# Optimization experiments

Hardware: AMD Instinct MI355X
Metric: run time of the kernel (lower is better)

Reference implementation:

```python
import jax, jax.numpy as jnp
import numpy as np

BT, HID, E, INTER, TOPK = 256, 2048, 8, 4096, 2

def setup_inputs() -> dict:
    key = jax.random.key(0)
    k1, k2, k3, k4, k5 = jax.random.split(key, 5)
    hidden_states = jax.random.normal(k1, (BT, HID), dtype=jnp.float32)
    expert_routing_table = jax.random.randint(k2, (BT, TOPK), 0, E, dtype=jnp.int64)
    router_weights = jax.random.uniform(k3, (BT, TOPK), dtype=jnp.float32)
    # learned params, scaled like trained weights
    w13_weight = jax.random.normal(k4, (E, 2 * INTER, HID), dtype=jnp.float32) * 0.02
    w2_weight = jax.random.normal(k5, (E, HID, INTER), dtype=jnp.float32) * 0.02
    return {
        "hidden_states": hidden_states,
        "expert_routing_table": expert_routing_table,
        "router_weights": router_weights,
        "w13_weight": w13_weight,
        "w2_weight": w2_weight,
    }

def reference(hidden_states, expert_routing_table, router_weights, w13_weight, w2_weight):
    bt, hidden_dim = hidden_states.shape
    num_experts = w13_weight.shape[0]
    inter = w2_weight.shape[2]
    sel = expert_routing_table  # [bt, top_k], ep_shift = 0
    # scatter router weights into dense [bt, E] (torch scatter_ set semantics)
    rows = jnp.arange(bt)[:, None]
    padded_weights = jnp.zeros((bt, num_experts), dtype=hidden_states.dtype)
    padded_weights = padded_weights.at[rows, sel].set(router_weights)
    # dense per-expert up/gate projection: [bt, E, 2*inter]
    up_gate = jnp.einsum('th,efh->tef', hidden_states, w13_weight)
    up_gate = up_gate.reshape(bt, num_experts, 2, inter)
    up_states = up_gate[:, :, 0, :]
    gate_states = up_gate[:, :, 1, :]
    cur = jax.nn.silu(up_states) * gate_states  # [bt, E, inter]
    # down projection + masked routed-weight sum over experts
    down = jnp.einsum('tei,ehi->teh', cur, w2_weight)  # [bt, E, hidden]
    final = jnp.einsum('teh,te->th', down, padded_weights)
    return final.reshape(-1, hidden_dim)
```

## Files before the change

### kernel.cpp

```cpp
#include <hip/hip_runtime.h>

#define BT 256
#define HID 2048
#define NE 8
#define INTER 4096

typedef short short8 __attribute__((ext_vector_type(8)));
typedef float f32x4 __attribute__((ext_vector_type(4)));

__device__ inline unsigned short f2bf(float f){
  unsigned int u = __float_as_uint(f);
  u += 0x7fff + ((u >> 16) & 1);
  return (unsigned short)(u >> 16);
}
__device__ inline unsigned int pk2(float x, float y){
  return (unsigned int)f2bf(x) | ((unsigned int)f2bf(y) << 16);
}
__device__ inline short8 cvt8(float4 a, float4 b){
  union { unsigned int u[4]; short8 s; } r;
  r.u[0] = pk2(a.x, a.y); r.u[1] = pk2(a.z, a.w);
  r.u[2] = pk2(b.x, b.y); r.u[3] = pk2(b.z, b.w);
  return r.s;
}

__device__ inline void glds16(const void* g, void* l){
  __builtin_amdgcn_global_load_lds(
      (const __attribute__((address_space(1))) unsigned int*)g,
      (__attribute__((address_space(3))) unsigned int*)l, 16, 0, 0);
}

__device__ inline short8 fragf(const float* tile, int row, int kbase){
  int cp = (kbase >> 3) ^ (row & 7);
  const float4* p = (const float4*)(tile + row*64 + cp*8);
  return cvt8(p[0], p[1]);
}
__device__ inline short8 fragh(const unsigned short* tile, int row, int kbase){
  int cp = (kbase >> 3) ^ (row & 7);
  return *(const short8*)(tile + row*64 + cp*8);
}

__global__ void routing_kernel(const int* __restrict__ sel, const float* __restrict__ rw,
                               int* counts, int* bases, int* tokl, float* wtl){
  __shared__ int cnt[NE]; __shared__ int bs[NE]; __shared__ int cur[NE];
  int t = threadIdx.x;
  if (t < NE) cnt[t] = 0;
  __syncthreads();
  int s0 = sel[2*t], s1 = sel[2*t+1];
  float w0 = rw[2*t], w1 = rw[2*t+1];
  bool dup = (s0 == s1);
  atomicAdd(&cnt[s1], 1);
  if (!dup) atomicAdd(&cnt[s0], 1);
  __syncthreads();
  if (t == 0){ int a = 0; for (int e = 0; e < NE; e++){ bs[e] = a; cur[e] = a; a += cnt[e]; } }
  __syncthreads();
  int slot = atomicAdd(&cur[s1], 1); tokl[slot] = t; wtl[slot] = w1;
  if (!dup){ slot = atomicAdd(&cur[s0], 1); tokl[slot] = t; wtl[slot] = w0; }
  if (t < NE){ counts[t] = cnt[t]; bases[t] = bs[t]; }
}

__global__ __launch_bounds__(256, 3) void gemm1_kernel(
    const float* __restrict__ hs, const float* __restrict__ w13,
    const int* __restrict__ counts, const int* __restrict__ bases,
    const int* __restrict__ tokl, unsigned short* __restrict__ cur)
{
  const int e = blockIdx.z;
  const int cnt = counts[e];
  const int mtile = blockIdx.y;
  if (mtile * 64 >= cnt) return;
  const int f0 = blockIdx.x * 64;
  const int base = bases[e];
  const int tid = threadIdx.x;

  __shared__ __align__(16) float As[64*64];
  __shared__ __align__(16) float Bs[128*64];

  const float* gA[4]; int offA[4];
#pragma unroll
  for (int r = 0; r < 4; r++){
    int off = r*4096 + tid*16;
    int row = off >> 8, b = off & 255;
    int cp = b >> 5, half = (b >> 4) & 1;
    int col = ((cp ^ (row & 7)) * 8) + half*4;
    int slot = mtile*64 + row; if (slot >= cnt) slot = cnt - 1;
    gA[r] = hs + (size_t)tokl[base + slot] * HID + col;
    offA[r] = off;
  }
  const float* gB[8]; int offB[8];
#pragma unroll
  for (int r = 0; r < 8; r++){
    int off = r*4096 + tid*16;
    int row = off >> 8, b = off & 255;
    int cp = b >> 5, half = (b >> 4) & 1;
    int col = ((cp ^ (row & 7)) * 8) + half*4;
    int wrow = (row < 64) ? (f0 + row) : (INTER + f0 + row - 64);
    gB[r] = w13 + (size_t)e * 2*INTER*HID + (size_t)wrow * HID + col;
    offB[r] = off;
  }

  const int wv = tid >> 6, wm = wv >> 1, wn = wv & 1;
  const int lane = tid & 63;
  const int lrow = lane & 15, quad = lane >> 4;

  f32x4 acc[2][2][2];
#pragma unroll
  for (int s=0;s<2;s++) for (int mt=0;mt<2;mt++) for (int nt=0;nt<2;nt++)
    acc[s][mt][nt] = (f32x4){0.f,0.f,0.f,0.f};

  for (int k0 = 0; k0 < HID; k0 += 64){
#pragma unroll
    for (int r = 0; r < 4; r++) glds16(gA[r] + k0, (char*)As + offA[r]);
#pragma unroll
    for (int r = 0; r < 8; r++) glds16(gB[r] + k0, (char*)Bs + offB[r]);
    __syncthreads();
#pragma unroll
    for (int ks = 0; ks < 64; ks += 32){
      int kb = ks + quad*8;
      short8 a[2], bb[2][2];
#pragma unroll
      for (int mt=0;mt<2;mt++) a[mt] = fragf(As, wm*32 + mt*16 + lrow, kb);
#pragma unroll
      for (int s=0;s<2;s++)
#pragma unroll
        for (int nt=0;nt<2;nt++)
          bb[s][nt] = fragf(Bs, s*64 + wn*32 + nt*16 + lrow, kb);
#pragma unroll
      for (int s=0;s<2;s++)
#pragma unroll
        for (int mt=0;mt<2;mt++)
#pragma unroll
          for (int nt=0;nt<2;nt++)
            acc[s][mt][nt] = __builtin_amdgcn_mfma_f32_16x16x32_bf16(
                a[mt], bb[s][nt], acc[s][mt][nt], 0,0,0);
    }
    __syncthreads();
  }

#pragma unroll
  for (int mt = 0; mt < 2; mt++){
#pragma unroll
    for (int reg = 0; reg < 4; reg++){
      int m = mtile*64 + wm*32 + mt*16 + quad*4 + reg;
      if (m >= cnt) continue;
      size_t rowoff = (size_t)(base + m) * INTER;
#pragma unroll
      for (int nt = 0; nt < 2; nt++){
        int i = f0 + wn*32 + nt*16 + lrow;
        float up   = acc[0][mt][nt][reg];
        float gate = acc[1][mt][nt][reg];
        float sv = up / (1.f + __expf(-up));
        cur[rowoff + i] = f2bf(sv * gate);
      }
    }
  }
}

__global__ __launch_bounds__(256, 4) void gemm2_kernel(
    const unsigned short* __restrict__ cur, const float* __restrict__ w2,
    const int* __restrict__ counts, const int* __restrict__ bases,
    const int* __restrict__ tokl, const float* __restrict__ wtl,
    float* __restrict__ out)
{
  const int e  = blockIdx.z >> 1;
  const int kb0 = (blockIdx.z & 1) * 2048;
  const int cnt = counts[e];
  const int mtile = blockIdx.y;
  if (mtile * 64 >= cnt) return;
  const int h0 = blockIdx.x * 32;
  const int base = bases[e];
  const int tid = threadIdx.x;

  __shared__ __align__(16) unsigned short Ah[64*64];
  __shared__ __align__(16) float Bs[32*64];

  const unsigned short* gA[2]; int offA[2];
#pragma unroll
  for (int r = 0; r < 2; r++){
    int off = r*4096 + tid*16;
    int row = off >> 7;
    int cp = (off >> 4) & 7;
    int col = (cp ^ (row & 7)) * 8;
    int slot = mtile*64 + row; if (slot >= cnt) slot = cnt - 1;
    gA[r] = cur + (size_t)(base + slot) * INTER + kb0 + col;
    offA[r] = off;
  }
  const float* gB[2]; int offB[2];
#pragma unroll
  for (int r = 0; r < 2; r++){
    int off = r*4096 + tid*16;
    int row = off >> 8, b = off & 255;
    int cp = b >> 5, half = (b >> 4) & 1;
    int col = ((cp ^ (row & 7)) * 8) + half*4;
    gB[r] = w2 + (size_t)e * HID * INTER + (size_t)(h0 + row) * INTER + kb0 + col;
    offB[r] = off;
  }

  const int wv = tid >> 6, wm = wv >> 1, wn = wv & 1;
  const int lane = tid & 63;
  const int lrow = lane & 15, quad = lane >> 4;

  f32x4 acc[2];
  acc[0] = (f32x4){0.f,0.f,0.f,0.f};
  acc[1] = (f32x4){0.f,0.f,0.f,0.f};

  for (int k0 = 0; k0 < 2048; k0 += 64){
#pragma unroll
    for (int r = 0; r < 2; r++) glds16(gA[r] + k0, (char*)Ah + offA[r]);
#pragma unroll
    for (int r = 0; r < 2; r++) glds16(gB[r] + k0, (char*)Bs + offB[r]);
    __syncthreads();
#pragma unroll
    for (int ks = 0; ks < 64; ks += 32){
      int kb = ks + quad*8;
      short8 a[2], b;
#pragma unroll
      for (int mt=0;mt<2;mt++) a[mt] = fragh(Ah, wm*32 + mt*16 + lrow, kb);
      b = fragf(Bs, wn*16 + lrow, kb);
#pragma unroll
      for (int mt=0;mt<2;mt++)
        acc[mt] = __builtin_amdgcn_mfma_f32_16x16x32_bf16(a[mt], b, acc[mt], 0,0,0);
    }
    __syncthreads();
  }

#pragma unroll
  for (int mt = 0; mt < 2; mt++){
#pragma unroll
    for (int reg = 0; reg < 4; reg++){
      int m = mtile*64 + wm*32 + mt*16 + quad*4 + reg;
      if (m >= cnt) continue;
      int tk  = tokl[base + m];
      float w = wtl[base + m];
      int h = h0 + wn*16 + lrow;
      atomicAdd(&out[(size_t)tk * HID + h], w * acc[mt][reg]);
    }
  }
}

extern "C" void kernel_launch(void* const* d_in, const int* in_sizes, int n_in,
                              void* d_out, int out_size, void* d_ws, size_t ws_size,
                              hipStream_t stream){
  const float* hs  = (const float*)d_in[0];
  const int*   sel = (const int*)d_in[1];
  const float* rw  = (const float*)d_in[2];
  const float* w13 = (const float*)d_in[3];
  const float* w2  = (const float*)d_in[4];
  float* out = (float*)d_out;
  char* ws = (char*)d_ws;

  int* counts = (int*)ws;
  int* bases  = counts + 8;
  int* tokl   = bases + 8;
  float* wtl  = (float*)(tokl + 512);
  unsigned short* cur = (unsigned short*)(ws + 8192);

  hipMemsetAsync(d_out, 0, (size_t)BT * HID * sizeof(float), stream);
  routing_kernel<<<1, 256, 0, stream>>>(sel, rw, counts, bases, tokl, wtl);
  dim3 g1(INTER/64, 4, NE);
  gemm1_kernel<<<g1, 256, 0, stream>>>(hs, w13, counts, bases, tokl, cur);
  dim3 g2(HID/32, 4, NE*2);
  gemm2_kernel<<<g2, 256, 0, stream>>>(cur, w2, counts, bases, tokl, wtl, out);
}
```

Measured before the change: 924.7 us.

## Pre-gather bf16 activations, double-buffer GEMM k-loops, enlarge M tiles to 128

A new gather kernel copies the routed token rows into a contiguous bf16 buffer, so gemm1 loads compact bf16 A tiles instead of indirect fp32 rows. Both GEMMs now use 128-row M tiles with k-step 32 and a two-stage LDS double buffer, using explicit vmcnt waits and raw barriers so loads overlap MFMA work. gemm2 drops the K split and computes 64-wide H tiles, which halves the atomic traffic per output element. In exchange there is an extra launch, lower occupancy, and row reads past cnt that rely on workspace padding.

```diff
diff --git a/kernel.cpp b/kernel.cpp
--- a/kernel.cpp
+++ b/kernel.cpp
@@ -12,6 +12,9 @@
   unsigned int u = __float_as_uint(f);
   u += 0x7fff + ((u >> 16) & 1);
   return (unsigned short)(u >> 16);
+}
+__device__ inline ushort4 f2bf4(float4 v){
+  ushort4 b; b.x=f2bf(v.x); b.y=f2bf(v.y); b.z=f2bf(v.z); b.w=f2bf(v.w); return b;
 }
 __device__ inline unsigned int pk2(float x, float y){
   return (unsigned int)f2bf(x) | ((unsigned int)f2bf(y) << 16);
@@ -29,15 +32,8 @@
       (__attribute__((address_space(3))) unsigned int*)l, 16, 0, 0);
 }
 
-__device__ inline short8 fragf(const float* tile, int row, int kbase){
-  int cp = (kbase >> 3) ^ (row & 7);
-  const float4* p = (const float4*)(tile + row*64 + cp*8);
-  return cvt8(p[0], p[1]);
-}
-__device__ inline short8 fragh(const unsigned short* tile, int row, int kbase){
-  int cp = (kbase >> 3) ^ (row & 7);
-  return *(const short8*)(tile + row*64 + cp*8);
-}
+#define WAIT_BARRIER(N) asm volatile("s_waitcnt vmcnt(" #N ")\n\ts_barrier" ::: "memory")
+#define RAW_BARRIER()   asm volatile("s_barrier" ::: "memory")
 
 __global__ void routing_kernel(const int* __restrict__ sel, const float* __restrict__ rw,
                                int* counts, int* bases, int* tokl, float* wtl){
@@ -58,88 +54,121 @@
   if (t < NE){ counts[t] = cnt[t]; bases[t] = bs[t]; }
 }
 
-__global__ __launch_bounds__(256, 3) void gemm1_kernel(
-    const float* __restrict__ hs, const float* __restrict__ w13,
+__global__ void gather_kernel(const float* __restrict__ hs,
+                              const int* __restrict__ counts, const int* __restrict__ bases,
+                              const int* __restrict__ tokl, unsigned short* __restrict__ hsg){
+  int b = blockIdx.x;
+  int tot = bases[NE-1] + counts[NE-1];
+  if (b >= tot) return;
+  const float* src = hs + (size_t)tokl[b] * HID;
+  unsigned short* dst = hsg + (size_t)b * HID;
+  int t = threadIdx.x;
+  float4 v0 = *(const float4*)(src + t*8);
+  float4 v1 = *(const float4*)(src + t*8 + 4);
+  *(ushort4*)(dst + t*8)     = f2bf4(v0);
+  *(ushort4*)(dst + t*8 + 4) = f2bf4(v1);
+}
+
+__global__ __launch_bounds__(256, 2) void gemm1_kernel(
+    const unsigned short* __restrict__ hsg, const float* __restrict__ w13,
     const int* __restrict__ counts, const int* __restrict__ bases,
-    const int* __restrict__ tokl, unsigned short* __restrict__ cur)
+    unsigned short* __restrict__ cur)
 {
   const int e = blockIdx.z;
   const int cnt = counts[e];
   const int mtile = blockIdx.y;
-  if (mtile * 64 >= cnt) return;
+  if (mtile * 128 >= cnt) return;
   const int f0 = blockIdx.x * 64;
   const int base = bases[e];
   const int tid = threadIdx.x;
 
-  __shared__ __align__(16) float As[64*64];
-  __shared__ __align__(16) float Bs[128*64];
-
-  const float* gA[4]; int offA[4];
+  __shared__ __align__(16) unsigned short Abuf[2][128*32];
+  __shared__ __align__(16) float          Bbuf[2][128*32];
+
+  const unsigned short* aG[2]; int aL[2];
+#pragma unroll
+  for (int r = 0; r < 2; r++){
+    int off = r*4096 + tid*16;
+    int row = off >> 6;
+    int gpos = (off >> 4) & 3;
+    int gglob = gpos ^ ((row >> 1) & 3);
+    aG[r] = hsg + (size_t)(base + mtile*128 + row) * HID + gglob*8;
+    aL[r] = off;
+  }
+  const float* bG[4]; int bL[4];
+  const size_t ebase = (size_t)e * 2*INTER*HID;
 #pragma unroll
   for (int r = 0; r < 4; r++){
     int off = r*4096 + tid*16;
-    int row = off >> 8, b = off & 255;
-    int cp = b >> 5, half = (b >> 4) & 1;
-    int col = ((cp ^ (row & 7)) * 8) + half*4;
-    int slot = mtile*64 + row; if (slot >= cnt) slot = cnt - 1;
-    gA[r] = hs + (size_t)tokl[base + slot] * HID + col;
-    offA[r] = off;
-  }
-  const float* gB[8]; int offB[8];
-#pragma unroll
-  for (int r = 0; r < 8; r++){
-    int off = r*4096 + tid*16;
-    int row = off >> 8, b = off & 255;
-    int cp = b >> 5, half = (b >> 4) & 1;
-    int col = ((cp ^ (row & 7)) * 8) + half*4;
+    int row = off >> 7;
+    int gpos = (off >> 4) & 7;
+    int gglob = gpos ^ (row & 7);
     int wrow = (row < 64) ? (f0 + row) : (INTER + f0 + row - 64);
-    gB[r] = w13 + (size_t)e * 2*INTER*HID + (size_t)wrow * HID + col;
-    offB[r] = off;
+    bG[r] = w13 + ebase + (size_t)wrow * HID + gglob*4;
+    bL[r] = off;
   }
 
   const int wv = tid >> 6, wm = wv >> 1, wn = wv & 1;
   const int lane = tid & 63;
   const int lrow = lane & 15, quad = lane >> 4;
 
-  f32x4 acc[2][2][2];
-#pragma unroll
-  for (int s=0;s<2;s++) for (int mt=0;mt<2;mt++) for (int nt=0;nt<2;nt++)
+  f32x4 acc[2][4][2];
+#pragma unroll
+  for (int s=0;s<2;s++) for (int mt=0;mt<4;mt++) for (int nt=0;nt<2;nt++)
     acc[s][mt][nt] = (f32x4){0.f,0.f,0.f,0.f};
 
-  for (int k0 = 0; k0 < HID; k0 += 64){
-#pragma unroll
-    for (int r = 0; r < 4; r++) glds16(gA[r] + k0, (char*)As + offA[r]);
-#pragma unroll
-    for (int r = 0; r < 8; r++) glds16(gB[r] + k0, (char*)Bs + offB[r]);
-    __syncthreads();
-#pragma unroll
-    for (int ks = 0; ks < 64; ks += 32){
-      int kb = ks + quad*8;
-      short8 a[2], bb[2][2];
-#pragma unroll
-      for (int mt=0;mt<2;mt++) a[mt] = fragf(As, wm*32 + mt*16 + lrow, kb);
-#pragma unroll
-      for (int s=0;s<2;s++)
-#pragma unroll
-        for (int nt=0;nt<2;nt++)
-          bb[s][nt] = fragf(Bs, s*64 + wn*32 + nt*16 + lrow, kb);
-#pragma unroll
-      for (int s=0;s<2;s++)
-#pragma unroll
-        for (int mt=0;mt<2;mt++)
-#pragma unroll
-          for (int nt=0;nt<2;nt++)
-            acc[s][mt][nt] = __builtin_amdgcn_mfma_f32_16x16x32_bf16(
-                a[mt], bb[s][nt], acc[s][mt][nt], 0,0,0);
-    }
-    __syncthreads();
-  }
-
-#pragma unroll
-  for (int mt = 0; mt < 2; mt++){
+  auto issue = [&](int t2, int p){
+    int k0 = t2 * 32;
+#pragma unroll
+    for (int r = 0; r < 2; r++) glds16(aG[r] + k0, (char*)&Abuf[p][0] + aL[r]);
+#pragma unroll
+    for (int r = 0; r < 4; r++) glds16(bG[r] + k0, (char*)&Bbuf[p][0] + bL[r]);
+  };
+  auto compute = [&](int p){
+    const unsigned short* A = &Abuf[p][0];
+    const float* B = &Bbuf[p][0];
+    short8 a[4], b[2][2];
+#pragma unroll
+    for (int mt = 0; mt < 4; mt++){
+      int row = wm*64 + mt*16 + lrow;
+      a[mt] = *(const short8*)(A + row*32 + ((quad ^ ((row>>1)&3)) * 8));
+    }
+#pragma unroll
+    for (int s = 0; s < 2; s++)
+#pragma unroll
+      for (int nt = 0; nt < 2; nt++){
+        int row = s*64 + wn*32 + nt*16 + lrow;
+        int g0 = (2*quad) ^ (row & 7), g1 = (2*quad+1) ^ (row & 7);
+        float4 x = *(const float4*)(B + row*32 + g0*4);
+        float4 y = *(const float4*)(B + row*32 + g1*4);
+        b[s][nt] = cvt8(x, y);
+      }
+#pragma unroll
+    for (int s = 0; s < 2; s++)
+#pragma unroll
+      for (int mt = 0; mt < 4; mt++)
+#pragma unroll
+        for (int nt = 0; nt < 2; nt++)
+          acc[s][mt][nt] = __builtin_amdgcn_mfma_f32_16x16x32_bf16(
+              a[mt], b[s][nt], acc[s][mt][nt], 0,0,0);
+  };
+
+  const int T = HID / 32;
+  issue(0, 0); issue(1, 1);
+  for (int t = 0; t < T-1; t++){
+    WAIT_BARRIER(6);
+    compute(t & 1);
+    RAW_BARRIER();
+    if (t + 2 < T) issue(t + 2, t & 1);
+  }
+  WAIT_BARRIER(0);
+  compute((T-1) & 1);
+
+#pragma unroll
+  for (int mt = 0; mt < 4; mt++){
 #pragma unroll
     for (int reg = 0; reg < 4; reg++){
-      int m = mtile*64 + wm*32 + mt*16 + quad*4 + reg;
+      int m = mtile*128 + wm*64 + mt*16 + quad*4 + reg;
       if (m >= cnt) continue;
       size_t rowoff = (size_t)(base + m) * INTER;
 #pragma unroll
@@ -154,84 +183,109 @@
   }
 }
 
-__global__ __launch_bounds__(256, 4) void gemm2_kernel(
+__global__ __launch_bounds__(256, 2) void gemm2_kernel(
     const unsigned short* __restrict__ cur, const float* __restrict__ w2,
     const int* __restrict__ counts, const int* __restrict__ bases,
     const int* __restrict__ tokl, const float* __restrict__ wtl,
     float* __restrict__ out)
 {
-  const int e  = blockIdx.z >> 1;
-  const int kb0 = (blockIdx.z & 1) * 2048;
+  const int e = blockIdx.z;
   const int cnt = counts[e];
   const int mtile = blockIdx.y;
-  if (mtile * 64 >= cnt) return;
-  const int h0 = blockIdx.x * 32;
+  if (mtile * 128 >= cnt) return;
+  const int h0 = blockIdx.x * 64;
   const int base = bases[e];
   const int tid = threadIdx.x;
 
-  __shared__ __align__(16) unsigned short Ah[64*64];
-  __shared__ __align__(16) float Bs[32*64];
-
-  const unsigned short* gA[2]; int offA[2];
+  __shared__ __align__(16) unsigned short Abuf[2][128*32];
+  __shared__ __align__(16) float          Bbuf[2][64*32];
+
+  const unsigned short* aG[2]; int aL[2];
+#pragma unroll
+  for (int r = 0; r < 2; r++){
+    int off = r*4096 + tid*16;
+    int row = off >> 6;
+    int gpos = (off >> 4) & 3;
+    int gglob = gpos ^ ((row >> 1) & 3);
+    aG[r] = cur + (size_t)(base + mtile*128 + row) * INTER + gglob*8;
+    aL[r] = off;
+  }
+  const float* bG[2]; int bL[2];
+  const size_t ebase = (size_t)e * HID * INTER;
 #pragma unroll
   for (int r = 0; r < 2; r++){
     int off = r*4096 + tid*16;
     int row = off >> 7;
-    int cp = (off >> 4) & 7;
-    int col = (cp ^ (row & 7)) * 8;
-    int slot = mtile*64 + row; if (slot >= cnt) slot = cnt - 1;
-    gA[r] = cur + (size_t)(base + slot) * INTER + kb0 + col;
-    offA[r] = off;
-  }
-  const float* gB[2]; int offB[2];
-#pragma unroll
-  for (int r = 0; r < 2; r++){
-    int off = r*4096 + tid*16;
-    int row = off >> 8, b = off & 255;
-    int cp = b >> 5, half = (b >> 4) & 1;
-    int col = ((cp ^ (row & 7)) * 8) + half*4;
-    gB[r] = w2 + (size_t)e * HID * INTER + (size_t)(h0 + row) * INTER + kb0 + col;
-    offB[r] = off;
+    int gpos = (off >> 4) & 7;
+    int gglob = gpos ^ (row & 7);
+    bG[r] = w2 + ebase + (size_t)(h0 + row) * INTER + gglob*4;
+    bL[r] = off;
   }
 
   const int wv = tid >> 6, wm = wv >> 1, wn = wv & 1;
   const int lane = tid & 63;
   const int lrow = lane & 15, quad = lane >> 4;
 
-  f32x4 acc[2];
-  acc[0] = (f32x4){0.f,0.f,0.f,0.f};
-  acc[1] = (f32x4){0.f,0.f,0.f,0.f};
-
-  for (int k0 = 0; k0 < 2048; k0 += 64){
-#pragma unroll
-    for (int r = 0; r < 2; r++) glds16(gA[r] + k0, (char*)Ah + offA[r]);
-#pragma unroll
-    for (int r = 0; r < 2; r++) glds16(gB[r] + k0, (char*)Bs + offB[r]);
-    __syncthreads();
-#pragma unroll
-    for (int ks = 0; ks < 64; ks += 32){
-      int kb = ks + quad*8;
-      short8 a[2], b;
-#pragma unroll
-      for (int mt=0;mt<2;mt++) a[mt] = fragh(Ah, wm*32 + mt*16 + lrow, kb);
-      b = fragf(Bs, wn*16 + lrow, kb);
-#pragma unroll
-      for (int mt=0;mt<2;mt++)
-        acc[mt] = __builtin_amdgcn_mfma_f32_16x16x32_bf16(a[mt], b, acc[mt], 0,0,0);
-    }
-    __syncthreads();
-  }
-
-#pragma unroll
-  for (int mt = 0; mt < 2; mt++){
+  f32x4 acc[4][2];
+#pragma unroll
+  for (int mt=0;mt<4;mt++) for (int nt=0;nt<2;nt++)
+    acc[mt][nt] = (f32x4){0.f,0.f,0.f,0.f};
+
+  auto issue = [&](int t2, int p){
+    int k0 = t2 * 32;
+#pragma unroll
+    for (int r = 0; r < 2; r++) glds16(aG[r] + k0, (char*)&Abuf[p][0] + aL[r]);
+#pragma unroll
+    for (int r = 0; r < 2; r++) glds16(bG[r] + k0, (char*)&Bbuf[p][0] + bL[r]);
+  };
+  auto compute = [&](int p){
+    const unsigned short* A = &Abuf[p][0];
+    const float* B = &Bbuf[p][0];
+    short8 a[4], b[2];
+#pragma unroll
+    for (int mt = 0; mt < 4; mt++){
+      int row = wm*64 + mt*16 + lrow;
+      a[mt] = *(const short8*)(A + row*32 + ((quad ^ ((row>>1)&3)) * 8));
+    }
+#pragma unroll
+    for (int nt = 0; nt < 2; nt++){
+      int row = wn*32 + nt*16 + lrow;
+      int g0 = (2*quad) ^ (row & 7), g1 = (2*quad+1) ^ (row & 7);
+      float4 x = *(const float4*)(B + row*32 + g0*4);
+      float4 y = *(const float4*)(B + row*32 + g1*4);
+      b[nt] = cvt8(x, y);
+    }
+#pragma unroll
+    for (int mt = 0; mt < 4; mt++)
+#pragma unroll
+      for (int nt = 0; nt < 2; nt++)
+        acc[mt][nt] = __builtin_amdgcn_mfma_f32_16x16x32_bf16(a[mt], b[nt], acc[mt][nt], 0,0,0);
+  };
+
+  const int T = INTER / 32;
+  issue(0, 0); issue(1, 1);
+  for (int t = 0; t < T-1; t++){
+    WAIT_BARRIER(4);
+    compute(t & 1);
+    RAW_BARRIER();
+    if (t + 2 < T) issue(t + 2, t & 1);
+  }
+  WAIT_BARRIER(0);
+  compute((T-1) & 1);
+
+#pragma unroll
+  for (int mt = 0; mt < 4; mt++){
 #pragma unroll
     for (int reg = 0; reg < 4; reg++){
-      int m = mtile*64 + wm*32 + mt*16 + quad*4 + reg;
+      int m = mtile*128 + wm*64 + mt*16 + quad*4 + reg;
       if (m >= cnt) continue;
       int tk  = tokl[base + m];
       float w = wtl[base + m];
-      int h = h0 + wn*16 + lrow;
-      atomicAdd(&out[(size_t)tk * HID + h], w * acc[mt][reg]);
+#pragma unroll
+      for (int nt = 0; nt < 2; nt++){
+        int h = h0 + wn*32 + nt*16 + lrow;
+        atomicAdd(&out[(size_t)tk * HID + h], w * acc[mt][nt][reg]);
+      }
     }
   }
 }
@@ -251,12 +305,14 @@
   int* bases  = counts + 8;
   int* tokl   = bases + 8;
   float* wtl  = (float*)(tokl + 512);
-  unsigned short* cur = (unsigned short*)(ws + 8192);
+  unsigned short* hsg = (unsigned short*)(ws + 8192);
+  unsigned short* cur = (unsigned short*)(ws + 8192 + 640*HID*2);
 
   hipMemsetAsync(d_out, 0, (size_t)BT * HID * sizeof(float), stream);
   routing_kernel<<<1, 256, 0, stream>>>(sel, rw, counts, bases, tokl, wtl);
-  dim3 g1(INTER/64, 4, NE);
-  gemm1_kernel<<<g1, 256, 0, stream>>>(hs, w13, counts, bases, tokl, cur);
-  dim3 g2(HID/32, 4, NE*2);
+  gather_kernel<<<512, 256, 0, stream>>>(hs, counts, bases, tokl, hsg);
+  dim3 g1(INTER/64, 2, NE);
+  gemm1_kernel<<<g1, 256, 0, stream>>>(hsg, w13, counts, bases, cur);
+  dim3 g2(HID/64, 2, NE);
   gemm2_kernel<<<g2, 256, 0, stream>>>(cur, w2, counts, bases, tokl, wtl, out);
 }
```

After: 966.9 us. +4.6%, slower.
